# Optimization experiments

Hardware: AMD Instinct MI355X
Metric: run time of the kernel (lower is better)

Reference implementation:

```python
import jax, jax.numpy as jnp
import numpy as np

KS = 3  # kernel_size


def _im2col(x):
    # x: (N, C, H, W) -> (N, H*W, C*KS*KS), matching torch unfold (channel-major,
    # kernel-position-minor) ordering with padding=1.
    N, C, H, W = x.shape
    xp = jnp.pad(x, ((0, 0), (0, 0), (1, 1), (1, 1)))
    patches = jnp.stack(
        [xp[:, :, i:i + H, j:j + W] for i in range(KS) for j in range(KS)],
        axis=2,
    )  # (N, C, 9, H, W)
    return patches.reshape(N, C * KS * KS, H * W).transpose(0, 2, 1)


def setup_inputs() -> dict:
    key = jax.random.key(0)
    k1, k2, k3, k4, k5 = jax.random.split(key, 5)
    N, C, H, W = 4, 64, 192, 192
    outC = 3
    return {
        "lr_features": jax.random.normal(k1, (N, C, H, W), dtype=jnp.float32),
        "W1": jax.random.normal(k2, (3, 256), dtype=jnp.float32) * 0.05,
        "b1": jax.random.normal(k3, (256,), dtype=jnp.float32) * 0.05,
        "W2": jax.random.normal(k4, (256, KS * KS * C * outC), dtype=jnp.float32) * 0.05,
        "b2": jax.random.normal(k5, (KS * KS * C * outC,), dtype=jnp.float32) * 0.05,
        "sr_scale": 4,
    }


def reference(lr_features, W1, b1, W2, b2, sr_scale):
    # Integer sr_scale: mask_mat is all-true and pos_mat_small is the s*s grid
    # of sub-pixel offsets [1/s, i/s, j/s] for i, j in [0, s).
    N, C, H, W = lr_features.shape
    s = int(np.ceil(sr_scale))
    inv = 1.0 / float(sr_scale)
    off = jnp.arange(s, dtype=jnp.float32) * inv
    pos = jnp.stack(jnp.meshgrid(off, off, indexing="ij"), axis=-1).reshape(s * s, 2)
    pos = jnp.concatenate(
        [jnp.full((s * s, 1), inv, dtype=jnp.float32), pos], axis=1
    )  # (s^2, 3)

    # Pos2Weight MLP -> per-subpixel dynamic conv weights (s^2, C*9, outC)
    hidden = jax.nn.relu(pos @ W1 + b1)
    local_weight = (hidden @ W2 + b2).reshape(s * s, KS * KS * C, -1)
    outC = local_weight.shape[-1]

    cols = _im2col(lr_features)  # (N, H*W, C*9)
    # batched small matmul: each sub-pixel position has its own filter
    out = jnp.einsum("npk,sko->nspo", cols, local_weight)  # (N, s^2, H*W, outC)
    out = out.reshape(N, s, s, H, W, outC)
    out = out.transpose(0, 5, 3, 1, 4, 2).reshape(N, outC, s * H, s * W)
    return out
```

## Files before the change

### kernel.cpp

```cpp
#include <hip/hip_runtime.h>


#define HH   192
#define WWD  192
#define SS   4
#define OC   3
#define PO   48
#define HID  256
#define W2LD 1728

typedef short  bf16x8 __attribute__((ext_vector_type(8)));
typedef float  f32x4  __attribute__((ext_vector_type(4)));

static __device__ __forceinline__ short f2bf(float f) {
    unsigned u = __float_as_uint(f);
    unsigned r = (u + 0x7fffu + ((u >> 16) & 1u)) >> 16;
    return (short)r;
}

static __device__ __forceinline__ void pin(bf16x8& v) {
    asm volatile("" : "+v"(v));
}

__global__ __launch_bounds__(256) void prep_kernel(
        const float* __restrict__ x,
        const float* __restrict__ W1, const float* __restrict__ b1,
        const float* __restrict__ W2, const float* __restrict__ b2,
        short* __restrict__ lwb, short* __restrict__ xt) {
    const int b = blockIdx.x;
    const int t = threadIdx.x;
    if (b < 112) {
        __shared__ float hlds[HID];
        const int p = b / 7;
        {
            const float pi = (float)(p >> 2) * 0.25f;
            const float pj = (float)(p & 3) * 0.25f;
            const float v = 0.25f * W1[t] + pi * W1[HID + t] + pj * W1[2 * HID + t]
                          + b1[t];
            hlds[t] = v > 0.f ? v : 0.f;
        }
        __syncthreads();
        const int col = (b % 7) * 256 + t;
        if (col < W2LD) {
            float a = 0.f;
#pragma unroll 32
            for (int hh = 0; hh < HID; ++hh)
                a += hlds[hh] * W2[hh * W2LD + col];
            const int o = col % 3, kc = col / 3;
            const int tap = kc % 9, c = kc / 9;
            lwb[(tap * PO + p * 3 + o) * 64 + c] = f2bf(a + b2[col]);
        }
    } else {
        __shared__ short tl[64][72];
        const int bb = b - 112;
        const int wt = bb % 3;
        const int h  = (bb / 3) % HH;
        const int n  = bb / (3 * HH);
        const int w0 = wt * 64;
#pragma unroll
        for (int i = 0; i < 4; ++i) {
            const int idx = i * 256 + t;
            const int c   = idx >> 4;
            const int j4  = idx & 15;
            const float4 v = *(const float4*)
                &x[(((size_t)(n * 64 + c)) * HH + h) * WWD + w0 + j4 * 4];
            tl[j4 * 4 + 0][c] = f2bf(v.x);
            tl[j4 * 4 + 1][c] = f2bf(v.y);
            tl[j4 * 4 + 2][c] = f2bf(v.z);
            tl[j4 * 4 + 3][c] = f2bf(v.w);
        }
        __syncthreads();
        const int w  = t >> 2;
        const int c0 = (t & 3) * 16;
        short* dst = &xt[(((size_t)n * HH + h) * WWD + w0 + w) * 64 + c0];
        *(bf16x8*)&dst[0] = *(const bf16x8*)&tl[w][c0];
        *(bf16x8*)&dst[8] = *(const bf16x8*)&tl[w][c0 + 8];
    }
}

__global__ __launch_bounds__(192, 3) void meta_up_mfma(
        const short* __restrict__ xt, const short* __restrict__ lwb,
        float* __restrict__ out) {
    __shared__ __align__(16) short smem[5 * 66 * 64];
    short* xlds = smem;
    float* obuf = (float*)smem;

    const int g   = (blockIdx.x & 7) * 96 + (blockIdx.x >> 3);
    const int n   = g / 192;
    const int rem = g % 192;
    const int wch = rem / 64;
    const int hg  = rem % 64;
    const int h0  = hg * 3;
    const int w0  = wch * 64;

    const int tid  = threadIdx.x;
    const int lane = tid & 63, wv = tid >> 6;
    const int quad = lane >> 4, l15 = lane & 15;

    {
        const bf16x8 z = {0, 0, 0, 0, 0, 0, 0, 0};
#pragma unroll
        for (int r0 = 0; r0 < 2; ++r0) {
            const int r = wv + r0 * 3;
            if (r >= 5) break;
            const int gr  = h0 - 1 + r;
            const bool rok = (unsigned)gr < (unsigned)HH;
            const short* __restrict__ src_row =
                xt + (size_t)(n * HH + (rok ? gr : 0)) * (WWD * 64);
            bf16x8 vv[8];
#pragma unroll
            for (int i = 0; i < 8; ++i) {
                const int q  = i * 64 + lane;
                const int j  = q >> 3, cb = q & 7;
                const int gc = w0 - 1 + j;
                const bool ok = rok && ((unsigned)gc < (unsigned)WWD);
                vv[i] = ok ?
                    *(const bf16x8*)&src_row[(size_t)(ok ? gc : 0) * 64 + cb * 8] : z;
            }
#pragma unroll
            for (int i = 0; i < 8; ++i) {
                const int q = i * 64 + lane;
                const int j = q >> 3, cb = q & 7;
                *(bf16x8*)&xlds[(r * 66 + j) * 64 + ((cb ^ (j & 7)) << 3)] = vv[i];
            }
            if (lane < 16) {
                const int q  = 512 + lane;
                const int j  = q >> 3, cb = q & 7;
                const int gc = w0 - 1 + j;
                const bool ok = rok && ((unsigned)gc < (unsigned)WWD);
                const bf16x8 v = ok ?
                    *(const bf16x8*)&src_row[(size_t)(ok ? gc : 0) * 64 + cb * 8] : z;
                *(bf16x8*)&xlds[(r * 66 + j) * 64 + ((cb ^ (j & 7)) << 3)] = v;
            }
        }
    }
    __syncthreads();

    f32x4 acc[3][4];
#pragma unroll
    for (int ih = 0; ih < 3; ++ih)
#pragma unroll
        for (int mt = 0; mt < 4; ++mt) acc[ih][mt] = (f32x4){0.f, 0.f, 0.f, 0.f};

    bf16x8 Bb[2][3];
#pragma unroll
    for (int di = 0; di < 3; ++di) {
        Bb[0][di] = *(const bf16x8*)
            &lwb[((di * 3 + 0) * PO + wv * 16 + l15) * 64 + 0 * 32 + quad * 8];
        pin(Bb[0][di]);
    }

#pragma unroll
    for (int b = 0; b < 6; ++b) {
        const int dj = b >> 1, kc2 = b & 1;
        if (b < 5) {
            const int djn = (b + 1) >> 1, kcn = (b + 1) & 1;
#pragma unroll
            for (int di = 0; di < 3; ++di) {
                Bb[(b + 1) & 1][di] = *(const bf16x8*)
                    &lwb[((di * 3 + djn) * PO + wv * 16 + l15) * 64 + kcn * 32 + quad * 8];
                pin(Bb[(b + 1) & 1][di]);
            }
        }
#pragma unroll
        for (int mt = 0; mt < 4; ++mt) {
            const int col = mt * 16 + l15 + dj;
            const int blk = (kc2 * 4 + quad) ^ (col & 7);
#pragma unroll
            for (int r = 0; r < 5; ++r) {
                bf16x8 a = *(const bf16x8*)&xlds[(r * 66 + col) * 64 + (blk << 3)];
#pragma unroll
                for (int di = 0; di < 3; ++di) {
                    const int ih = r - di;
                    if (ih >= 0 && ih < 3)
                        acc[ih][mt] = __builtin_amdgcn_mfma_f32_16x16x32_bf16(
                            a, Bb[b & 1][di], acc[ih][mt], 0, 0, 0);
                }
            }
        }
    }

    __syncthreads();
    {
        const int po = wv * 16 + l15;
        const int o  = po % 3;
        const int p  = po / 3;
        const int si = p >> 2, sj = p & 3;
        const int osi = o * 4 + si;
#pragma unroll
        for (int ih = 0; ih < 3; ++ih)
#pragma unroll
            for (int mt = 0; mt < 4; ++mt)
#pragma unroll
                for (int r4 = 0; r4 < 4; ++r4) {
                    const int wl = mt * 16 + quad * 4 + r4;
                    obuf[(ih * 12 + osi) * 260 + wl * 4 + sj] = acc[ih][mt][r4];
                }
    }
    __syncthreads();
    {
        const int osi = tid >> 4;
        const int c16 = tid & 15;
        const int o = osi >> 2, si = osi & 3;
#pragma unroll
        for (int ih = 0; ih < 3; ++ih) {
            const int hh = h0 + ih;
            const size_t base =
                ((size_t)(n * OC + o) * (SS * HH) + (size_t)(SS * hh + si)) * (SS * WWD)
                + (size_t)(4 * w0) + c16 * 16;
            const float* __restrict__ src = &obuf[(ih * 12 + osi) * 260 + c16 * 16];
#pragma unroll
            for (int i = 0; i < 4; ++i)
                *(float4*)&out[base + i * 4] = *(const float4*)&src[i * 4];
        }
    }
}

extern "C" void kernel_launch(void* const* d_in, const int* in_sizes, int n_in,
                              void* d_out, int out_size, void* d_ws, size_t ws_size,
                              hipStream_t stream) {
    const float* x  = (const float*)d_in[0];
    const float* W1 = (const float*)d_in[1];
    const float* b1 = (const float*)d_in[2];
    const float* W2 = (const float*)d_in[3];
    const float* b2 = (const float*)d_in[4];
    float* out = (float*)d_out;
    short* lwb = (short*)d_ws;
    short* xt  = (short*)d_ws + 32768;

    prep_kernel<<<112 + 4 * HH * 3, 256, 0, stream>>>(x, W1, b1, W2, b2, lwb, xt);
    meta_up_mfma<<<768, 192, 0, stream>>>(xt, lwb, out);
}
```

Before: 118.2 us.

## Fuse fp32-to-bf16 NHWC transpose into main MFMA kernel's LDS load

Removes the separate pass that converted the NCHW fp32 input into an NHWC bf16 buffer in workspace. The main kernel now reads fp32 input directly with per-channel strided loads, converts to bf16, packs 8 channels, and writes them into the swizzled LDS tile, using software-pipelined prefetch. It also reorders block-to-tile mapping so neighbouring blocks share rows. This avoids a round trip through global memory but uses strided, less-vectorised global reads and reloads halo rows redundantly across blocks.

Result: no change. 118.7 us (+0.5%).

```diff
diff --git a/kernel.cpp b/kernel.cpp
--- a/kernel.cpp
+++ b/kernel.cpp
@@ -22,64 +22,36 @@
     asm volatile("" : "+v"(v));
 }
 
-__global__ __launch_bounds__(256) void prep_kernel(
-        const float* __restrict__ x,
+__global__ __launch_bounds__(256) void lw_kernel(
         const float* __restrict__ W1, const float* __restrict__ b1,
         const float* __restrict__ W2, const float* __restrict__ b2,
-        short* __restrict__ lwb, short* __restrict__ xt) {
+        short* __restrict__ lwb) {
+    __shared__ float hlds[HID];
     const int b = blockIdx.x;
     const int t = threadIdx.x;
-    if (b < 112) {
-        __shared__ float hlds[HID];
-        const int p = b / 7;
-        {
-            const float pi = (float)(p >> 2) * 0.25f;
-            const float pj = (float)(p & 3) * 0.25f;
-            const float v = 0.25f * W1[t] + pi * W1[HID + t] + pj * W1[2 * HID + t]
-                          + b1[t];
-            hlds[t] = v > 0.f ? v : 0.f;
-        }
-        __syncthreads();
-        const int col = (b % 7) * 256 + t;
-        if (col < W2LD) {
-            float a = 0.f;
+    const int p = b / 7;
+    {
+        const float pi = (float)(p >> 2) * 0.25f;
+        const float pj = (float)(p & 3) * 0.25f;
+        const float v = 0.25f * W1[t] + pi * W1[HID + t] + pj * W1[2 * HID + t]
+                      + b1[t];
+        hlds[t] = v > 0.f ? v : 0.f;
+    }
+    __syncthreads();
+    const int col = (b % 7) * 256 + t;
+    if (col < W2LD) {
+        float a = 0.f;
 #pragma unroll 32
-            for (int hh = 0; hh < HID; ++hh)
-                a += hlds[hh] * W2[hh * W2LD + col];
-            const int o = col % 3, kc = col / 3;
-            const int tap = kc % 9, c = kc / 9;
-            lwb[(tap * PO + p * 3 + o) * 64 + c] = f2bf(a + b2[col]);
-        }
-    } else {
-        __shared__ short tl[64][72];
-        const int bb = b - 112;
-        const int wt = bb % 3;
-        const int h  = (bb / 3) % HH;
-        const int n  = bb / (3 * HH);
-        const int w0 = wt * 64;
-#pragma unroll
-        for (int i = 0; i < 4; ++i) {
-            const int idx = i * 256 + t;
-            const int c   = idx >> 4;
-            const int j4  = idx & 15;
-            const float4 v = *(const float4*)
-                &x[(((size_t)(n * 64 + c)) * HH + h) * WWD + w0 + j4 * 4];
-            tl[j4 * 4 + 0][c] = f2bf(v.x);
-            tl[j4 * 4 + 1][c] = f2bf(v.y);
-            tl[j4 * 4 + 2][c] = f2bf(v.z);
-            tl[j4 * 4 + 3][c] = f2bf(v.w);
-        }
-        __syncthreads();
-        const int w  = t >> 2;
-        const int c0 = (t & 3) * 16;
-        short* dst = &xt[(((size_t)n * HH + h) * WWD + w0 + w) * 64 + c0];
-        *(bf16x8*)&dst[0] = *(const bf16x8*)&tl[w][c0];
-        *(bf16x8*)&dst[8] = *(const bf16x8*)&tl[w][c0 + 8];
+        for (int hh = 0; hh < HID; ++hh)
+            a += hlds[hh] * W2[hh * W2LD + col];
+        const int o = col % 3, kc = col / 3;
+        const int tap = kc % 9, c = kc / 9;
+        lwb[(tap * PO + p * 3 + o) * 64 + c] = f2bf(a + b2[col]);
     }
 }
 
 __global__ __launch_bounds__(192, 3) void meta_up_mfma(
-        const short* __restrict__ xt, const short* __restrict__ lwb,
+        const float* __restrict__ x, const short* __restrict__ lwb,
         float* __restrict__ out) {
     __shared__ __align__(16) short smem[5 * 66 * 64];
     short* xlds = smem;
@@ -88,59 +60,14 @@
     const int g   = (blockIdx.x & 7) * 96 + (blockIdx.x >> 3);
     const int n   = g / 192;
     const int rem = g % 192;
-    const int wch = rem / 64;
-    const int hg  = rem % 64;
+    const int hg  = rem / 3;
+    const int wch = rem % 3;
     const int h0  = hg * 3;
     const int w0  = wch * 64;
 
     const int tid  = threadIdx.x;
     const int lane = tid & 63, wv = tid >> 6;
     const int quad = lane >> 4, l15 = lane & 15;
-
-    {
-        const bf16x8 z = {0, 0, 0, 0, 0, 0, 0, 0};
-#pragma unroll
-        for (int r0 = 0; r0 < 2; ++r0) {
-            const int r = wv + r0 * 3;
-            if (r >= 5) break;
-            const int gr  = h0 - 1 + r;
-            const bool rok = (unsigned)gr < (unsigned)HH;
-            const short* __restrict__ src_row =
-                xt + (size_t)(n * HH + (rok ? gr : 0)) * (WWD * 64);
-            bf16x8 vv[8];
-#pragma unroll
-            for (int i = 0; i < 8; ++i) {
-                const int q  = i * 64 + lane;
-                const int j  = q >> 3, cb = q & 7;
-                const int gc = w0 - 1 + j;
-                const bool ok = rok && ((unsigned)gc < (unsigned)WWD);
-                vv[i] = ok ?
-                    *(const bf16x8*)&src_row[(size_t)(ok ? gc : 0) * 64 + cb * 8] : z;
-            }
-#pragma unroll
-            for (int i = 0; i < 8; ++i) {
-                const int q = i * 64 + lane;
-                const int j = q >> 3, cb = q & 7;
-                *(bf16x8*)&xlds[(r * 66 + j) * 64 + ((cb ^ (j & 7)) << 3)] = vv[i];
-            }
-            if (lane < 16) {
-                const int q  = 512 + lane;
-                const int j  = q >> 3, cb = q & 7;
-                const int gc = w0 - 1 + j;
-                const bool ok = rok && ((unsigned)gc < (unsigned)WWD);
-                const bf16x8 v = ok ?
-                    *(const bf16x8*)&src_row[(size_t)(ok ? gc : 0) * 64 + cb * 8] : z;
-                *(bf16x8*)&xlds[(r * 66 + j) * 64 + ((cb ^ (j & 7)) << 3)] = v;
-            }
-        }
-    }
-    __syncthreads();
-
-    f32x4 acc[3][4];
-#pragma unroll
-    for (int ih = 0; ih < 3; ++ih)
-#pragma unroll
-        for (int mt = 0; mt < 4; ++mt) acc[ih][mt] = (f32x4){0.f, 0.f, 0.f, 0.f};
 
     bf16x8 Bb[2][3];
 #pragma unroll
@@ -149,6 +76,74 @@
             &lwb[((di * 3 + 0) * PO + wv * 16 + l15) * 64 + 0 * 32 + quad * 8];
         pin(Bb[0][di]);
     }
+
+    {
+        const int gc  = w0 - 1 + lane;
+        const bool cok = (unsigned)gc < (unsigned)WWD;
+        int ci = wv;
+        float cur[8];
+        {
+            const int r = ci >> 3, cb = ci & 7;
+            const int gr = h0 - 1 + r;
+            const bool ok = cok && ((unsigned)gr < (unsigned)HH);
+            const float* __restrict__ p = x +
+                ((size_t)(n * 64 + cb * 8) * HH + (ok ? gr : 0)) * WWD + (cok ? gc : 0);
+#pragma unroll
+            for (int cc = 0; cc < 8; ++cc)
+                cur[cc] = ok ? p[(size_t)cc * HH * WWD] : 0.f;
+        }
+#pragma unroll
+        for (int k = 0; k < 14; ++k) {
+            const int nx = ci + 3;
+            const bool more = (nx < 40);
+            float nxt[8];
+            if (more) {
+                const int r = nx >> 3, cb = nx & 7;
+                const int gr = h0 - 1 + r;
+                const bool ok = cok && ((unsigned)gr < (unsigned)HH);
+                const float* __restrict__ p = x +
+                    ((size_t)(n * 64 + cb * 8) * HH + (ok ? gr : 0)) * WWD + (cok ? gc : 0);
+#pragma unroll
+                for (int cc = 0; cc < 8; ++cc)
+                    nxt[cc] = ok ? p[(size_t)cc * HH * WWD] : 0.f;
+            }
+            {
+                const int r = ci >> 3, cb = ci & 7;
+                bf16x8 pk;
+#pragma unroll
+                for (int cc = 0; cc < 8; ++cc) pk[cc] = f2bf(cur[cc]);
+                *(bf16x8*)&xlds[(r * 66 + lane) * 64 + ((cb ^ (lane & 7)) << 3)] = pk;
+            }
+            if (!more) break;
+#pragma unroll
+            for (int cc = 0; cc < 8; ++cc) cur[cc] = nxt[cc];
+            ci = nx;
+        }
+        if (lane < 16) {
+            const int j  = 64 + (lane >> 3);
+            const int cb = lane & 7;
+            const int gc2 = w0 - 1 + j;
+            const bool cok2 = (unsigned)gc2 < (unsigned)WWD;
+            for (int r = wv; r < 5; r += 3) {
+                const int gr = h0 - 1 + r;
+                const bool ok = cok2 && ((unsigned)gr < (unsigned)HH);
+                const float* __restrict__ p = x +
+                    ((size_t)(n * 64 + cb * 8) * HH + (ok ? gr : 0)) * WWD + (cok2 ? gc2 : 0);
+                bf16x8 pk;
+#pragma unroll
+                for (int cc = 0; cc < 8; ++cc)
+                    pk[cc] = f2bf(ok ? p[(size_t)cc * HH * WWD] : 0.f);
+                *(bf16x8*)&xlds[(r * 66 + j) * 64 + ((cb ^ (j & 7)) << 3)] = pk;
+            }
+        }
+    }
+    __syncthreads();
+
+    f32x4 acc[3][4];
+#pragma unroll
+    for (int ih = 0; ih < 3; ++ih)
+#pragma unroll
+        for (int mt = 0; mt < 4; ++mt) acc[ih][mt] = (f32x4){0.f, 0.f, 0.f, 0.f};
 
 #pragma unroll
     for (int b = 0; b < 6; ++b) {
@@ -226,8 +221,7 @@
     const float* b2 = (const float*)d_in[4];
     float* out = (float*)d_out;
     short* lwb = (short*)d_ws;
-    short* xt  = (short*)d_ws + 32768;
-
-    prep_kernel<<<112 + 4 * HH * 3, 256, 0, stream>>>(x, W1, b1, W2, b2, lwb, xt);
-    meta_up_mfma<<<768, 192, 0, stream>>>(xt, lwb, out);
-}
+
+    lw_kernel<<<112, 256, 0, stream>>>(W1, b1, W2, b2, lwb);
+    meta_up_mfma<<<768, 192, 0, stream>>>(x, lwb, out);
+}
```

## Double waves per block by splitting column tiles across two wave groups

Applied to the files above, without the earlier changes.

Grows the main MFMA kernel from 3 to 6 waves per block. Each wave group handles half of the 64-column tile, so per-wave accumulators drop from 12 to 6 fragments. The LDS fill is flattened into a single strided loop over all 384 threads, the B-fragment prefetch is hoisted ahead of the fill, and the output store is redistributed as one float4 per thread per step. The aim is more latency hiding and fewer registers per wave. The cost is that each B fragment is now loaded by twice as many waves, and the launch-bounds occupancy hint is gone.

Measured after the change: 118.6 us. About the same (+0.3%).

```diff
diff --git a/kernel.cpp b/kernel.cpp
--- a/kernel.cpp
+++ b/kernel.cpp
@@ -78,7 +78,7 @@
     }
 }
 
-__global__ __launch_bounds__(192, 3) void meta_up_mfma(
+__global__ __launch_bounds__(384) void meta_up_mfma(
         const short* __restrict__ xt, const short* __restrict__ lwb,
         float* __restrict__ out) {
     __shared__ __align__(16) short smem[5 * 66 * 64];
@@ -94,53 +94,11 @@
     const int w0  = wch * 64;
 
     const int tid  = threadIdx.x;
-    const int lane = tid & 63, wv = tid >> 6;
+    const int lane = tid & 63;
+    const int wv   = (tid >> 6) % 3;
+    const int wg   = tid >> 7 >= 1 ? (tid >= 256 ? 1 : (tid >= 192 ? 1 : 0)) : 0;
+    const int wgq  = (tid >> 6) / 3;
     const int quad = lane >> 4, l15 = lane & 15;
-
-    {
-        const bf16x8 z = {0, 0, 0, 0, 0, 0, 0, 0};
-#pragma unroll
-        for (int r0 = 0; r0 < 2; ++r0) {
-            const int r = wv + r0 * 3;
-            if (r >= 5) break;
-            const int gr  = h0 - 1 + r;
-            const bool rok = (unsigned)gr < (unsigned)HH;
-            const short* __restrict__ src_row =
-                xt + (size_t)(n * HH + (rok ? gr : 0)) * (WWD * 64);
-            bf16x8 vv[8];
-#pragma unroll
-            for (int i = 0; i < 8; ++i) {
-                const int q  = i * 64 + lane;
-                const int j  = q >> 3, cb = q & 7;
-                const int gc = w0 - 1 + j;
-                const bool ok = rok && ((unsigned)gc < (unsigned)WWD);
-                vv[i] = ok ?
-                    *(const bf16x8*)&src_row[(size_t)(ok ? gc : 0) * 64 + cb * 8] : z;
-            }
-#pragma unroll
-            for (int i = 0; i < 8; ++i) {
-                const int q = i * 64 + lane;
-                const int j = q >> 3, cb = q & 7;
-                *(bf16x8*)&xlds[(r * 66 + j) * 64 + ((cb ^ (j & 7)) << 3)] = vv[i];
-            }
-            if (lane < 16) {
-                const int q  = 512 + lane;
-                const int j  = q >> 3, cb = q & 7;
-                const int gc = w0 - 1 + j;
-                const bool ok = rok && ((unsigned)gc < (unsigned)WWD);
-                const bf16x8 v = ok ?
-                    *(const bf16x8*)&src_row[(size_t)(ok ? gc : 0) * 64 + cb * 8] : z;
-                *(bf16x8*)&xlds[(r * 66 + j) * 64 + ((cb ^ (j & 7)) << 3)] = v;
-            }
-        }
-    }
-    __syncthreads();
-
-    f32x4 acc[3][4];
-#pragma unroll
-    for (int ih = 0; ih < 3; ++ih)
-#pragma unroll
-        for (int mt = 0; mt < 4; ++mt) acc[ih][mt] = (f32x4){0.f, 0.f, 0.f, 0.f};
 
     bf16x8 Bb[2][3];
 #pragma unroll
@@ -150,6 +108,34 @@
         pin(Bb[0][di]);
     }
 
+    {
+        const bf16x8 z = {0, 0, 0, 0, 0, 0, 0, 0};
+#pragma unroll
+        for (int k = 0; k < 7; ++k) {
+            const int item = k * 384 + tid;
+            if (item < 2640) {
+                const int r   = item / 528;
+                const int rm  = item - r * 528;
+                const int j   = rm >> 3;
+                const int cb  = rm & 7;
+                const int gr  = h0 - 1 + r;
+                const int gc  = w0 - 1 + j;
+                const bool ok = ((unsigned)gr < (unsigned)HH) &&
+                                ((unsigned)gc < (unsigned)WWD);
+                const bf16x8 v = ok ? *(const bf16x8*)
+                    &xt[((size_t)(n * HH + gr) * WWD + gc) * 64 + cb * 8] : z;
+                *(bf16x8*)&xlds[(r * 66 + j) * 64 + ((cb ^ (j & 7)) << 3)] = v;
+            }
+        }
+    }
+    __syncthreads();
+
+    f32x4 acc[3][2];
+#pragma unroll
+    for (int ih = 0; ih < 3; ++ih)
+#pragma unroll
+        for (int mtl = 0; mtl < 2; ++mtl) acc[ih][mtl] = (f32x4){0.f, 0.f, 0.f, 0.f};
+
 #pragma unroll
     for (int b = 0; b < 6; ++b) {
         const int dj = b >> 1, kc2 = b & 1;
@@ -163,7 +149,8 @@
             }
         }
 #pragma unroll
-        for (int mt = 0; mt < 4; ++mt) {
+        for (int mtl = 0; mtl < 2; ++mtl) {
+            const int mt  = wgq * 2 + mtl;
             const int col = mt * 16 + l15 + dj;
             const int blk = (kc2 * 4 + quad) ^ (col & 7);
 #pragma unroll
@@ -173,8 +160,8 @@
                 for (int di = 0; di < 3; ++di) {
                     const int ih = r - di;
                     if (ih >= 0 && ih < 3)
-                        acc[ih][mt] = __builtin_amdgcn_mfma_f32_16x16x32_bf16(
-                            a, Bb[b & 1][di], acc[ih][mt], 0, 0, 0);
+                        acc[ih][mtl] = __builtin_amdgcn_mfma_f32_16x16x32_bf16(
+                            a, Bb[b & 1][di], acc[ih][mtl], 0, 0, 0);
                 }
             }
         }
@@ -190,29 +177,32 @@
 #pragma unroll
         for (int ih = 0; ih < 3; ++ih)
 #pragma unroll
-            for (int mt = 0; mt < 4; ++mt)
+            for (int mtl = 0; mtl < 2; ++mtl) {
+                const int mt = wgq * 2 + mtl;
 #pragma unroll
                 for (int r4 = 0; r4 < 4; ++r4) {
                     const int wl = mt * 16 + quad * 4 + r4;
-                    obuf[(ih * 12 + osi) * 260 + wl * 4 + sj] = acc[ih][mt][r4];
+                    obuf[(ih * 12 + osi) * 260 + wl * 4 + sj] = acc[ih][mtl][r4];
                 }
+            }
     }
     __syncthreads();
     {
-        const int osi = tid >> 4;
-        const int c16 = tid & 15;
-        const int o = osi >> 2, si = osi & 3;
-#pragma unroll
-        for (int ih = 0; ih < 3; ++ih) {
-            const int hh = h0 + ih;
-            const size_t base =
-                ((size_t)(n * OC + o) * (SS * HH) + (size_t)(SS * hh + si)) * (SS * WWD)
-                + (size_t)(4 * w0) + c16 * 16;
-            const float* __restrict__ src = &obuf[(ih * 12 + osi) * 260 + c16 * 16];
-#pragma unroll
-            for (int i = 0; i < 4; ++i)
-                *(float4*)&out[base + i * 4] = *(const float4*)&src[i * 4];
-        }
+#pragma unroll
+        for (int ih = 0; ih < 3; ++ih)
+#pragma unroll
+            for (int h2 = 0; h2 < 2; ++h2) {
+                const int idx = h2 * 384 + tid;
+                const int osi = idx >> 6;
+                const int c4  = idx & 63;
+                const int o = osi >> 2, si = osi & 3;
+                const int hh = h0 + ih;
+                const size_t base =
+                    ((size_t)(n * OC + o) * (SS * HH) + (size_t)(SS * hh + si))
+                        * (SS * WWD) + (size_t)(4 * w0) + c4 * 4;
+                *(float4*)&out[base] =
+                    *(const float4*)&obuf[(ih * 12 + osi) * 260 + c4 * 4];
+            }
     }
 }
 
@@ -229,5 +219,5 @@
     short* xt  = (short*)d_ws + 32768;
 
     prep_kernel<<<112 + 4 * HH * 3, 256, 0, stream>>>(x, W1, b1, W2, b2, lwb, xt);
-    meta_up_mfma<<<768, 192, 0, stream>>>(xt, lwb, out);
-}
+    meta_up_mfma<<<768, 384, 0, stream>>>(xt, lwb, out);
+}
```
